# Optimization experiments

Measured on AMD Instinct MI355X. Metric: run time of the kernel, lower is better.

## Reference

```python
import jax, jax.numpy as jnp
import numpy as np

N, NFEAT, NHID, E = 100000, 256, 64, 1600000
EPS = 1e-5
NEG_SLOPE = 0.2


def _glorot(k, shape):
    lim = float(np.sqrt(6.0 / (shape[0] + shape[1])))
    return jax.random.uniform(k, shape, jnp.float32, -lim, lim)


def setup_inputs() -> dict:
    key = jax.random.key(0)
    ks = jax.random.split(key, 24)
    inp = {
        "g": jax.random.normal(ks[0], (N, NFEAT), jnp.float32),           # node features
        "x": jax.random.randint(ks[1], (2, E), 0, N),                      # edge_index [src; dst]
    }
    # estimator GAT params
    inp["est_W"] = _glorot(ks[2], (NFEAT, NHID))
    inp["est_asrc"] = _glorot(ks[3], (NHID, 1))[:, 0]
    inp["est_adst"] = _glorot(ks[4], (NHID, 1))[:, 0]
    inp["est_bias"] = jnp.zeros((NHID,), jnp.float32)
    inp["est_gamma"] = jnp.ones((NHID,), jnp.float32)
    inp["est_beta"] = jnp.zeros((NHID,), jnp.float32)
    inp["est_rmean"] = 0.1 * jax.random.normal(ks[5], (NHID,), jnp.float32)
    inp["est_rvar"] = jax.random.uniform(ks[6], (NHID,), jnp.float32, 0.5, 1.5)
    # GNN GAT params
    inp["gnn_W"] = _glorot(ks[7], (NFEAT, NHID))
    inp["gnn_asrc"] = _glorot(ks[8], (NHID, 1))[:, 0]
    inp["gnn_adst"] = _glorot(ks[9], (NHID, 1))[:, 0]
    inp["gnn_bias"] = jnp.zeros((NHID,), jnp.float32)
    inp["gnn_gamma"] = jnp.ones((NHID,), jnp.float32)
    inp["gnn_beta"] = jnp.zeros((NHID,), jnp.float32)
    inp["gnn_rmean"] = 0.1 * jax.random.normal(ks[10], (NHID,), jnp.float32)
    inp["gnn_rvar"] = jax.random.uniform(ks[11], (NHID,), jnp.float32, 0.5, 1.5)
    # classifier head
    inp["cls_W"] = _glorot(ks[12], (NHID, 1))
    inp["cls_b"] = jnp.zeros((1,), jnp.float32)
    return inp


def _gat(feat, src, dst, W, a_src, a_dst, bias, gamma, beta, rmean, rvar):
    # GATConv (heads=1): linear -> per-edge attention logits -> segment softmax over dst -> weighted scatter
    h = feat @ W                                  # [N, NHID]
    e_src = h @ a_src                             # [N]
    e_dst = h @ a_dst                             # [N]
    e = jax.nn.leaky_relu(e_src[src] + e_dst[dst], NEG_SLOPE)   # [E+N]
    m = jax.ops.segment_max(e, dst, num_segments=N)
    p = jnp.exp(e - m[dst])
    z = jax.ops.segment_sum(p, dst, num_segments=N)
    alpha = p / z[dst]                            # softmax per destination node
    out = jax.ops.segment_sum(h[src] * alpha[:, None], dst, num_segments=N) + bias
    # transition: ReLU -> BatchNorm1d (eval, running stats) -> Dropout (identity in eval)
    out = jnp.maximum(out, 0.0)
    return (out - rmean) * jax.lax.rsqrt(rvar + EPS) * gamma + beta


def reference(g, x, est_W, est_asrc, est_adst, est_bias, est_gamma, est_beta, est_rmean, est_rvar,
              gnn_W, gnn_asrc, gnn_adst, gnn_bias, gnn_gamma, gnn_beta, gnn_rmean, gnn_rvar,
              cls_W, cls_b):
    loop = jnp.arange(N)                          # add_self_loops=True
    src = jnp.concatenate([x[0], loop])
    dst = jnp.concatenate([x[1], loop])
    s = _gat(g, src, dst, est_W, est_asrc, est_adst, est_bias, est_gamma, est_beta, est_rmean, est_rvar)
    z = _gat(g, src, dst, gnn_W, gnn_asrc, gnn_adst, gnn_bias, gnn_gamma, gnn_beta, gnn_rmean, gnn_rvar)
    y = z @ cls_W + cls_b                         # [N, 1]
    return (y, s)
```

## Files before the change

kernel.cpp:

```cpp
#include <hip/hip_runtime.h>
#include <math.h>
#include <float.h>

#define NFEAT 256
#define NHID 64
#define BN_EPS 1e-5f

typedef float f32x4 __attribute__((ext_vector_type(4)));
typedef short s16x8 __attribute__((ext_vector_type(8)));

__device__ __forceinline__ float lrelu(float x) { return x >= 0.f ? x : 0.2f * x; }
__device__ __forceinline__ unsigned short f2bf(float f) {
    unsigned int u = __float_as_uint(f);
    return (unsigned short)((u + 0x7fffu + ((u >> 16) & 1u)) >> 16);
}
__device__ __forceinline__ float bf_lo(unsigned int v) { return __uint_as_float(v << 16); }
__device__ __forceinline__ float bf_hi(unsigned int v) { return __uint_as_float(v & 0xffff0000u); }

__global__ void prep_w_k(const float* __restrict__ We, const float* __restrict__ Wg,
                         unsigned short* __restrict__ Wt) {
    int tid = blockIdx.x * 256 + threadIdx.x;
    int ks  = tid >> 12;
    int col = (tid >> 5) & 127;
    int kk  = tid & 31;
    int k   = ks * 32 + kk;
    float v = (col < 64) ? We[k * 64 + col] : Wg[k * 64 + (col - 64)];
    size_t byte = (size_t)ks * 10240 + col * 80 + (kk >> 3) * 16 + (kk & 7) * 2;
    Wt[byte >> 1] = f2bf(v);
}

__global__ void bucket_hist_k(const int* __restrict__ x, int E, int* __restrict__ bcnt) {
    __shared__ int lh[256];
    int tid = threadIdx.x;
    lh[tid] = 0;
    __syncthreads();
    int base = (blockIdx.x * 256 + tid) * 8;
    if (base + 8 <= E) {
        int4 d0 = *(const int4*)(x + E + base);
        int4 d1 = *(const int4*)(x + E + base + 4);
        atomicAdd(&lh[d0.x >> 9], 1); atomicAdd(&lh[d0.y >> 9], 1);
        atomicAdd(&lh[d0.z >> 9], 1); atomicAdd(&lh[d0.w >> 9], 1);
        atomicAdd(&lh[d1.x >> 9], 1); atomicAdd(&lh[d1.y >> 9], 1);
        atomicAdd(&lh[d1.z >> 9], 1); atomicAdd(&lh[d1.w >> 9], 1);
    } else {
        for (int k = 0; k < 8; ++k)
            if (base + k < E) atomicAdd(&lh[x[E + base + k] >> 9], 1);
    }
    __syncthreads();
    if (lh[tid] > 0) atomicAdd(&bcnt[tid], lh[tid]);
}

__global__ void bucket_scan_k(const int* __restrict__ bcnt, int M, int NBKT,
                              int* __restrict__ bucket_base, int* __restrict__ bcursor,
                              int* __restrict__ csr_base) {
    __shared__ int s_c[2][256], s_t[2][256];
    int tid = threadIdx.x;
    int c = (tid < NBKT) ? bcnt[tid] : 0;
    int n0 = tid << 9;
    int sc = (tid < NBKT) ? min(512, M - n0) : 0;
    int tot = c + sc;
    s_c[0][tid] = c; s_t[0][tid] = tot;
    __syncthreads();
    int cur = 0;
    for (int off = 1; off < 256; off <<= 1) {
        int nc = s_c[cur][tid] + (tid >= off ? s_c[cur][tid - off] : 0);
        int nt = s_t[cur][tid] + (tid >= off ? s_t[cur][tid - off] : 0);
        s_c[cur ^ 1][tid] = nc; s_t[cur ^ 1][tid] = nt;
        __syncthreads();
        cur ^= 1;
    }
    if (tid < NBKT) {
        int eb = s_c[cur][tid] - c;
        bucket_base[tid] = eb;
        bcursor[tid] = eb;
        csr_base[tid] = s_t[cur][tid] - tot;
    }
}

__global__ void bucket_scatter_k(const int* __restrict__ x, int E,
                                 int* __restrict__ bcursor, int* __restrict__ ebuf) {
    __shared__ int lh[256], gb[256];
    int tid = threadIdx.x;
    lh[tid] = 0;
    __syncthreads();
    int base = (blockIdx.x * 256 + tid) * 8;
    int pk[8], bk[8], rk[8];
    bool v[8];
    if (base + 8 <= E) {
        int4 s0 = *(const int4*)(x + base);
        int4 s1 = *(const int4*)(x + base + 4);
        int4 d0 = *(const int4*)(x + E + base);
        int4 d1 = *(const int4*)(x + E + base + 4);
        int ss[8] = {s0.x, s0.y, s0.z, s0.w, s1.x, s1.y, s1.z, s1.w};
        int dd[8] = {d0.x, d0.y, d0.z, d0.w, d1.x, d1.y, d1.z, d1.w};
#pragma unroll
        for (int k = 0; k < 8; ++k) {
            v[k] = true;
            bk[k] = dd[k] >> 9;
            pk[k] = ((dd[k] & 511) << 17) | ss[k];
        }
    } else {
#pragma unroll
        for (int k = 0; k < 8; ++k) {
            int i = base + k;
            v[k] = (i < E);
            if (v[k]) {
                int s = x[i], d = x[E + i];
                bk[k] = d >> 9;
                pk[k] = ((d & 511) << 17) | s;
            } else { bk[k] = 0; pk[k] = 0; }
        }
    }
#pragma unroll
    for (int k = 0; k < 8; ++k)
        if (v[k]) rk[k] = atomicAdd(&lh[bk[k]], 1);
    __syncthreads();
    if (lh[tid] > 0) gb[tid] = atomicAdd(&bcursor[tid], lh[tid]);
    __syncthreads();
#pragma unroll
    for (int k = 0; k < 8; ++k)
        if (v[k]) ebuf[gb[bk[k]] + rk[k]] = pk[k];
}

__global__ __launch_bounds__(256) void bucket_csr_k(const int* __restrict__ bcnt,
                                                    const int* __restrict__ bucket_base,
                                                    const int* __restrict__ csr_base,
                                                    const int* __restrict__ ebuf, int M,
                                                    int* __restrict__ row_start,
                                                    int* __restrict__ deg,
                                                    int* __restrict__ srcs) {
    int b = blockIdx.x, tid = threadIdx.x;
    int nE = bcnt[b];
    int ebase = bucket_base[b];
    int cbase = csr_base[b];
    int n0 = b << 9;
    int nloc = min(512, M - n0);
    __shared__ int cnt[512], sa[512], sb[512], cur[512];
#pragma unroll
    for (int k = 0; k < 2; ++k) {
        int i = tid + k * 256;
        cnt[i] = (i < nloc) ? 1 : 0;
    }
    __syncthreads();
    for (int j = tid; j < nE; j += 256)
        atomicAdd(&cnt[ebuf[ebase + j] >> 17], 1);
    __syncthreads();
#pragma unroll
    for (int k = 0; k < 2; ++k) { int i = tid + k * 256; sa[i] = cnt[i]; }
    __syncthreads();
    int* a = sa; int* bb = sb;
    for (int off = 1; off < 512; off <<= 1) {
#pragma unroll
        for (int k = 0; k < 2; ++k) {
            int i = tid + k * 256;
            bb[i] = a[i] + (i >= off ? a[i - off] : 0);
        }
        __syncthreads();
        int* t = a; a = bb; bb = t;
    }
#pragma unroll
    for (int k = 0; k < 2; ++k) {
        int i = tid + k * 256;
        int excl = a[i] - cnt[i];
        cur[i] = excl;
        if (i < nloc) {
            row_start[n0 + i] = cbase + excl;
            deg[n0 + i] = cnt[i];
            srcs[cbase + excl] = n0 + i;
            cur[i] = excl + 1;
        }
    }
    __syncthreads();
    for (int j = tid; j < nE; j += 256) {
        int p = ebuf[ebase + j];
        int dl = p >> 17, src = p & 0x1FFFF;
        int pos = atomicAdd(&cur[dl], 1);
        srcs[cbase + pos] = src;
    }
}

__global__ __launch_bounds__(256) void gemm_mfma_k(const float* __restrict__ g,
                                                   const char* __restrict__ Wt,
                                                   unsigned short* __restrict__ hh,
                                                   const float* __restrict__ ase,
                                                   const float* __restrict__ ade,
                                                   const float* __restrict__ asg,
                                                   const float* __restrict__ adg,
                                                   float2* __restrict__ esrc,
                                                   float2* __restrict__ edst, int M) {
    __shared__ __align__(16) char lds[21504];
    char* As = lds;
    char* Bs = lds + 10240;
    float* av = (float*)(lds + 20480);
    const int tid = threadIdx.x;
    const int l = tid & 63;
    const int w = tid >> 6;
    const int row0 = blockIdx.x * 128;

    {
        float v;
        if (tid < 64)       v = ase[tid];
        else if (tid < 128) v = ade[tid - 64];
        else if (tid < 192) v = asg[tid - 128];
        else                v = adg[tid - 192];
        av[tid] = v;
    }

    f32x4 acc[2][8];
#pragma unroll
    for (int r = 0; r < 2; r++)
#pragma unroll
        for (int n = 0; n < 8; n++) acc[r][n] = (f32x4){0.f, 0.f, 0.f, 0.f};

    const int arow = tid >> 1;
    const int ah = tid & 1;

    for (int ks = 0; ks < 8; ++ks) {
        {
            int grow = row0 + arow;
            float4 v0 = {0,0,0,0}, v1 = v0, v2 = v0, v3 = v0;
            if (grow < M) {
                const float* gp = g + (size_t)grow * NFEAT + ks * 32 + ah * 16;
                v0 = *(const float4*)(gp + 0);
                v1 = *(const float4*)(gp + 4);
                v2 = *(const float4*)(gp + 8);
                v3 = *(const float4*)(gp + 12);
            }
            s16x8 c0, c1;
            c0[0]=f2bf(v0.x); c0[1]=f2bf(v0.y); c0[2]=f2bf(v0.z); c0[3]=f2bf(v0.w);
            c0[4]=f2bf(v1.x); c0[5]=f2bf(v1.y); c0[6]=f2bf(v1.z); c0[7]=f2bf(v1.w);
            c1[0]=f2bf(v2.x); c1[1]=f2bf(v2.y); c1[2]=f2bf(v2.z); c1[3]=f2bf(v2.w);
            c1[4]=f2bf(v3.x); c1[5]=f2bf(v3.y); c1[6]=f2bf(v3.z); c1[7]=f2bf(v3.w);
            *(s16x8*)(As + arow * 80 + ah * 32)      = c0;
            *(s16x8*)(As + arow * 80 + ah * 32 + 16) = c1;
        }
        {
            const char* wp = Wt + (size_t)ks * 10240 + arow * 80 + ah * 32;
            *(s16x8*)(Bs + arow * 80 + ah * 32)      = *(const s16x8*)(wp);
            *(s16x8*)(Bs + arow * 80 + ah * 32 + 16) = *(const s16x8*)(wp + 16);
        }
        __syncthreads();
        s16x8 af[2];
#pragma unroll
        for (int r = 0; r < 2; r++)
            af[r] = *(const s16x8*)(As + (w * 32 + r * 16 + (l & 15)) * 80 + (l >> 4) * 16);
#pragma unroll
        for (int n = 0; n < 8; n++) {
            s16x8 bf = *(const s16x8*)(Bs + (n * 16 + (l & 15)) * 80 + (l >> 4) * 16);
            acc[0][n] = __builtin_amdgcn_mfma_f32_16x16x32_bf16(af[0], bf, acc[0][n], 0, 0, 0);
            acc[1][n] = __builtin_amdgcn_mfma_f32_16x16x32_bf16(af[1], bf, acc[1][n], 0, 0, 0);
        }
        __syncthreads();
    }

    float vs_e[4], vd_e[4], vs_g[4], vd_g[4];
    {
        const int l16 = l & 15;
#pragma unroll
        for (int n = 0; n < 4; ++n) {
            vs_e[n] = av[n * 16 + l16];
            vd_e[n] = av[64 + n * 16 + l16];
            vs_g[n] = av[128 + n * 16 + l16];
            vd_g[n] = av[192 + n * 16 + l16];
        }
    }

    unsigned short* epi = (unsigned short*)lds;
#pragma unroll
    for (int p = 0; p < 2; ++p) {
        {
            float pse[4] = {0,0,0,0}, pde[4] = {0,0,0,0};
            float psg[4] = {0,0,0,0}, pdg[4] = {0,0,0,0};
#pragma unroll
            for (int n = 0; n < 4; ++n)
#pragma unroll
                for (int j = 0; j < 4; ++j) {
                    float he = acc[p][n][j];
                    float hg = acc[p][n + 4][j];
                    pse[j] += he * vs_e[n];
                    pde[j] += he * vd_e[n];
                    psg[j] += hg * vs_g[n];
                    pdg[j] += hg * vd_g[n];
                }
#pragma unroll
            for (int off = 1; off <= 8; off <<= 1) {
#pragma unroll
                for (int j = 0; j < 4; ++j) {
                    pse[j] += __shfl_xor(pse[j], off, 64);
                    pde[j] += __shfl_xor(pde[j], off, 64);
                    psg[j] += __shfl_xor(psg[j], off, 64);
                    pdg[j] += __shfl_xor(pdg[j], off, 64);
                }
            }
            if ((l & 15) == 0) {
#pragma unroll
                for (int j = 0; j < 4; ++j) {
                    int gr = row0 + w * 32 + p * 16 + (l >> 4) * 4 + j;
                    if (gr < M) {
                        esrc[gr] = make_float2(pse[j], psg[j]);
                        edst[gr] = make_float2(pde[j], pdg[j]);
                    }
                }
            }
        }
#pragma unroll
        for (int n = 0; n < 8; n++)
#pragma unroll
            for (int j = 0; j < 4; j++)
                epi[(w * 16 + (l >> 4) * 4 + j) * 128 + n * 16 + (l & 15)] = f2bf(acc[p][n][j]);
        __syncthreads();
        int er = tid >> 2, sgm = tid & 3;
        int grow2 = row0 + 32 * (er >> 4) + 16 * p + (er & 15);
        if (grow2 < M) {
            const s16x8* src = (const s16x8*)(epi + er * 128 + sgm * 32);
            s16x8* dst = (s16x8*)(hh + (size_t)grow2 * 128 + sgm * 32);
#pragma unroll
            for (int q = 0; q < 4; q++) dst[q] = src[q];
        }
        __syncthreads();
    }
}

__global__ void node_acc_k(const int* __restrict__ srcs, const int* __restrict__ row_start,
                           const int* __restrict__ deg,
                           const float2* __restrict__ esrc, const float2* __restrict__ edst,
                           const unsigned short* __restrict__ hh,
                           const float* __restrict__ be, const float* __restrict__ ge,
                           const float* __restrict__ bte, const float* __restrict__ rme,
                           const float* __restrict__ rve,
                           const float* __restrict__ bg, const float* __restrict__ gg,
                           const float* __restrict__ btg, const float* __restrict__ rmg,
                           const float* __restrict__ rvg,
                           const float* __restrict__ clsW, const float* __restrict__ clsb,
                           float* __restrict__ y, float* __restrict__ s_out, int M) {
    int n = blockIdx.x * 4 + (threadIdx.x >> 6);
    int l = threadIdx.x & 63;
    if (n >= M) return;
    int beg = row_start[n];
    int cnt = deg[n];
    int eh = l >> 5;
    int li = l & 31;
    int layer = li >> 4;
    float2 ed = edst[n];
    float edv = layer ? ed.y : ed.x;
    const int* sp = srcs + beg;
    const char* hb = (const char*)hh + (unsigned)li * 8;
    float a0 = 0.f, a1 = 0.f, a2 = 0.f, a3 = 0.f, zacc = 0.f;
    int j = 0;
    for (; j + 8 <= cnt; j += 8) {
        int s[4];
#pragma unroll
        for (int k = 0; k < 4; ++k) s[k] = sp[j + 2 * k + eh];
        float2 e[4];
        uint2 h[4];
#pragma unroll
        for (int k = 0; k < 4; ++k) e[k] = esrc[s[k]];
#pragma unroll
        for (int k = 0; k < 4; ++k)
            h[k] = *(const uint2*)(hb + ((size_t)(unsigned)s[k] << 8));
#pragma unroll
        for (int k = 0; k < 4; ++k) {
            float a = __expf(lrelu((layer ? e[k].y : e[k].x) + edv));
            zacc += a;
            a0 += a * bf_lo(h[k].x); a1 += a * bf_hi(h[k].x);
            a2 += a * bf_lo(h[k].y); a3 += a * bf_hi(h[k].y);
        }
    }
    for (; j < cnt; j += 2) {
        int idx = j + eh;
        if (idx < cnt) {
            int s = sp[idx];
            float2 e = esrc[s];
            uint2 h = *(const uint2*)(hb + ((size_t)(unsigned)s << 8));
            float a = __expf(lrelu((layer ? e.y : e.x) + edv));
            zacc += a;
            a0 += a * bf_lo(h.x); a1 += a * bf_hi(h.x);
            a2 += a * bf_lo(h.y); a3 += a * bf_hi(h.y);
        }
    }
    a0 += __shfl_xor(a0, 32, 64);
    a1 += __shfl_xor(a1, 32, 64);
    a2 += __shfl_xor(a2, 32, 64);
    a3 += __shfl_xor(a3, 32, 64);
    zacc += __shfl_xor(zacc, 32, 64);
    float rz = 1.f / zacc;
    float o0 = a0 * rz, o1 = a1 * rz, o2 = a2 * rz, o3 = a3 * rz;

    int c16 = li & 15;
    float4 b4  = layer ? ((const float4*)bg)[c16]  : ((const float4*)be)[c16];
    float4 rm4 = layer ? ((const float4*)rmg)[c16] : ((const float4*)rme)[c16];
    float4 rv4 = layer ? ((const float4*)rvg)[c16] : ((const float4*)rve)[c16];
    float4 g4  = layer ? ((const float4*)gg)[c16]  : ((const float4*)ge)[c16];
    float4 bt4 = layer ? ((const float4*)btg)[c16] : ((const float4*)bte)[c16];
    o0 = (fmaxf(o0 + b4.x, 0.f) - rm4.x) * rsqrtf(rv4.x + BN_EPS) * g4.x + bt4.x;
    o1 = (fmaxf(o1 + b4.y, 0.f) - rm4.y) * rsqrtf(rv4.y + BN_EPS) * g4.y + bt4.y;
    o2 = (fmaxf(o2 + b4.z, 0.f) - rm4.z) * rsqrtf(rv4.z + BN_EPS) * g4.z + bt4.z;
    o3 = (fmaxf(o3 + b4.w, 0.f) - rm4.w) * rsqrtf(rv4.w + BN_EPS) * g4.w + bt4.w;

    if (eh == 0) {
        if (layer == 0) {
            float4 sv = {o0, o1, o2, o3};
            ((float4*)(s_out + (size_t)n * 64))[c16] = sv;
        } else {
            float4 w4 = ((const float4*)clsW)[c16];
            float t = o0 * w4.x + o1 * w4.y + o2 * w4.z + o3 * w4.w;
#pragma unroll
            for (int off = 1; off <= 8; off <<= 1) t += __shfl_xor(t, off, 64);
            if (li == 16) y[n] = t + clsb[0];
        }
    }
}

extern "C" void kernel_launch(void* const* d_in, const int* in_sizes, int n_in,
                              void* d_out, int out_size, void* d_ws, size_t ws_size,
                              hipStream_t stream) {
    const float* g        = (const float*)d_in[0];
    const int*   x        = (const int*)d_in[1];
    const float* est_W    = (const float*)d_in[2];
    const float* est_asrc = (const float*)d_in[3];
    const float* est_adst = (const float*)d_in[4];
    const float* est_bias = (const float*)d_in[5];
    const float* est_gamma= (const float*)d_in[6];
    const float* est_beta = (const float*)d_in[7];
    const float* est_rmean= (const float*)d_in[8];
    const float* est_rvar = (const float*)d_in[9];
    const float* gnn_W    = (const float*)d_in[10];
    const float* gnn_asrc = (const float*)d_in[11];
    const float* gnn_adst = (const float*)d_in[12];
    const float* gnn_bias = (const float*)d_in[13];
    const float* gnn_gamma= (const float*)d_in[14];
    const float* gnn_beta = (const float*)d_in[15];
    const float* gnn_rmean= (const float*)d_in[16];
    const float* gnn_rvar = (const float*)d_in[17];
    const float* cls_W    = (const float*)d_in[18];
    const float* cls_b    = (const float*)d_in[19];

    const int M  = in_sizes[0] / NFEAT;
    const int E  = in_sizes[1] / 2;
    const int Et = E + M;
    const int NBKT = (M + 511) >> 9;

    float* y_out = (float*)d_out;
    float* s_out = y_out + M;

    char* base = (char*)d_ws;
    unsigned short* hh = (unsigned short*)base;
    size_t off = (size_t)M * 128 * 2;
    char* Wt = base + off;                  off += 81920;
    float2* esrc = (float2*)(base + off);   off += (size_t)M * 8;
    float2* edst = (float2*)(base + off);   off += (size_t)M * 8;
    int* deg       = (int*)(base + off);    off += (size_t)M * 4;
    int* row_start = (int*)(base + off);    off += (size_t)M * 4;
    int* srcs      = (int*)(base + off);    off += (size_t)Et * 4;
    int* ebuf      = (int*)(base + off);    off += (size_t)E * 4;
    int* bcnt        = (int*)(base + off);  off += 256 * 4;
    int* bucket_base = (int*)(base + off);  off += 256 * 4;
    int* bcursor     = (int*)(base + off);  off += 256 * 4;
    int* csr_base    = (int*)(base + off);  off += 256 * 4;

    const int EB = (E + 2047) / 2048;

    prep_w_k<<<128, 256, 0, stream>>>(est_W, gnn_W, (unsigned short*)Wt);
    hipMemsetAsync(bcnt, 0, 256 * 4, stream);
    bucket_hist_k<<<EB, 256, 0, stream>>>(x, E, bcnt);
    bucket_scan_k<<<1, 256, 0, stream>>>(bcnt, M, NBKT, bucket_base, bcursor, csr_base);
    bucket_scatter_k<<<EB, 256, 0, stream>>>(x, E, bcursor, ebuf);
    bucket_csr_k<<<NBKT, 256, 0, stream>>>(bcnt, bucket_base, csr_base, ebuf, M,
                                           row_start, deg, srcs);

    gemm_mfma_k<<<(M + 127) / 128, 256, 0, stream>>>(g, Wt, hh,
                                                     est_asrc, est_adst, gnn_asrc, gnn_adst,
                                                     esrc, edst, M);

    node_acc_k<<<(M + 3) / 4, 256, 0, stream>>>(srcs, row_start, deg, esrc, edst, hh,
                                                est_bias, est_gamma, est_beta, est_rmean, est_rvar,
                                                gnn_bias, gnn_gamma, gnn_beta, gnn_rmean, gnn_rvar,
                                                cls_W, cls_b, y_out, s_out, M);
}
```

Before: 201.1 us.

## Precompute per-edge attention weights during CSR construction and reorder GEMM first

Moves the GEMM ahead of the CSR build so that bucket_csr_k can compute exp(leaky_relu(esrc+edst)) for both layers per edge. It writes these into a new CSR-ordered pa array. node_acc_k then streams pa sequentially instead of gathering esrc randomly and recomputing exp. This replaces a random 8-byte gather per edge with a coalesced read, but adds a random esrc gather and extra 8-byte writes in the CSR kernel.

```diff
diff --git a/kernel.cpp b/kernel.cpp
--- a/kernel.cpp
+++ b/kernel.cpp
@@ -126,9 +126,12 @@
                                                     const int* __restrict__ bucket_base,
                                                     const int* __restrict__ csr_base,
                                                     const int* __restrict__ ebuf, int M,
+                                                    const float2* __restrict__ esrc,
+                                                    const float2* __restrict__ edst,
                                                     int* __restrict__ row_start,
                                                     int* __restrict__ deg,
-                                                    int* __restrict__ srcs) {
+                                                    int* __restrict__ srcs,
+                                                    float2* __restrict__ pa) {
     int b = blockIdx.x, tid = threadIdx.x;
     int nE = bcnt[b];
     int ebase = bucket_base[b];
@@ -136,10 +139,12 @@
     int n0 = b << 9;
     int nloc = min(512, M - n0);
     __shared__ int cnt[512], sa[512], sb[512], cur[512];
+    __shared__ float2 edl[512];
 #pragma unroll
     for (int k = 0; k < 2; ++k) {
         int i = tid + k * 256;
         cnt[i] = (i < nloc) ? 1 : 0;
+        edl[i] = (i < nloc) ? edst[n0 + i] : make_float2(0.f, 0.f);
     }
     __syncthreads();
     for (int j = tid; j < nE; j += 256)
@@ -167,6 +172,10 @@
             row_start[n0 + i] = cbase + excl;
             deg[n0 + i] = cnt[i];
             srcs[cbase + excl] = n0 + i;
+            float2 es = esrc[n0 + i];
+            float2 ed = edl[i];
+            pa[cbase + excl] = make_float2(__expf(lrelu(es.x + ed.x)),
+                                           __expf(lrelu(es.y + ed.y)));
             cur[i] = excl + 1;
         }
     }
@@ -176,6 +185,10 @@
         int dl = p >> 17, src = p & 0x1FFFF;
         int pos = atomicAdd(&cur[dl], 1);
         srcs[cbase + pos] = src;
+        float2 es = esrc[src];
+        float2 ed = edl[dl];
+        pa[cbase + pos] = make_float2(__expf(lrelu(es.x + ed.x)),
+                                      __expf(lrelu(es.y + ed.y)));
     }
 }
 
@@ -322,8 +335,7 @@
 }
 
 __global__ void node_acc_k(const int* __restrict__ srcs, const int* __restrict__ row_start,
-                           const int* __restrict__ deg,
-                           const float2* __restrict__ esrc, const float2* __restrict__ edst,
+                           const int* __restrict__ deg, const float2* __restrict__ pa,
                            const unsigned short* __restrict__ hh,
                            const float* __restrict__ be, const float* __restrict__ ge,
                            const float* __restrict__ bte, const float* __restrict__ rme,
@@ -341,26 +353,25 @@
     int eh = l >> 5;
     int li = l & 31;
     int layer = li >> 4;
-    float2 ed = edst[n];
-    float edv = layer ? ed.y : ed.x;
     const int* sp = srcs + beg;
+    const float2* pp = pa + beg;
     const char* hb = (const char*)hh + (unsigned)li * 8;
     float a0 = 0.f, a1 = 0.f, a2 = 0.f, a3 = 0.f, zacc = 0.f;
     int j = 0;
     for (; j + 8 <= cnt; j += 8) {
         int s[4];
+        float2 pv[4];
+        uint2 h[4];
 #pragma unroll
         for (int k = 0; k < 4; ++k) s[k] = sp[j + 2 * k + eh];
-        float2 e[4];
-        uint2 h[4];
-#pragma unroll
-        for (int k = 0; k < 4; ++k) e[k] = esrc[s[k]];
+#pragma unroll
+        for (int k = 0; k < 4; ++k) pv[k] = pp[j + 2 * k + eh];
 #pragma unroll
         for (int k = 0; k < 4; ++k)
             h[k] = *(const uint2*)(hb + ((size_t)(unsigned)s[k] << 8));
 #pragma unroll
         for (int k = 0; k < 4; ++k) {
-            float a = __expf(lrelu((layer ? e[k].y : e[k].x) + edv));
+            float a = layer ? pv[k].y : pv[k].x;
             zacc += a;
             a0 += a * bf_lo(h[k].x); a1 += a * bf_hi(h[k].x);
             a2 += a * bf_lo(h[k].y); a3 += a * bf_hi(h[k].y);
@@ -370,9 +381,9 @@
         int idx = j + eh;
         if (idx < cnt) {
             int s = sp[idx];
-            float2 e = esrc[s];
+            float2 pv = pp[idx];
             uint2 h = *(const uint2*)(hb + ((size_t)(unsigned)s << 8));
-            float a = __expf(lrelu((layer ? e.y : e.x) + edv));
+            float a = layer ? pv.y : pv.x;
             zacc += a;
             a0 += a * bf_lo(h.x); a1 += a * bf_hi(h.x);
             a2 += a * bf_lo(h.y); a3 += a * bf_hi(h.y);
@@ -452,6 +463,7 @@
     int* deg       = (int*)(base + off);    off += (size_t)M * 4;
     int* row_start = (int*)(base + off);    off += (size_t)M * 4;
     int* srcs      = (int*)(base + off);    off += (size_t)Et * 4;
+    float2* pa     = (float2*)(base + off); off += (size_t)Et * 8;
     int* ebuf      = (int*)(base + off);    off += (size_t)E * 4;
     int* bcnt        = (int*)(base + off);  off += 256 * 4;
     int* bucket_base = (int*)(base + off);  off += 256 * 4;
@@ -461,18 +473,18 @@
     const int EB = (E + 2047) / 2048;
 
     prep_w_k<<<128, 256, 0, stream>>>(est_W, gnn_W, (unsigned short*)Wt);
+    gemm_mfma_k<<<(M + 127) / 128, 256, 0, stream>>>(g, Wt, hh,
+                                                     est_asrc, est_adst, gnn_asrc, gnn_adst,
+                                                     esrc, edst, M);
+
     hipMemsetAsync(bcnt, 0, 256 * 4, stream);
     bucket_hist_k<<<EB, 256, 0, stream>>>(x, E, bcnt);
     bucket_scan_k<<<1, 256, 0, stream>>>(bcnt, M, NBKT, bucket_base, bcursor, csr_base);
     bucket_scatter_k<<<EB, 256, 0, stream>>>(x, E, bcursor, ebuf);
     bucket_csr_k<<<NBKT, 256, 0, stream>>>(bcnt, bucket_base, csr_base, ebuf, M,
-                                           row_start, deg, srcs);
-
-    gemm_mfma_k<<<(M + 127) / 128, 256, 0, stream>>>(g, Wt, hh,
-                                                     est_asrc, est_adst, gnn_asrc, gnn_adst,
-                                                     esrc, edst, M);
-
-    node_acc_k<<<(M + 3) / 4, 256, 0, stream>>>(srcs, row_start, deg, esrc, edst, hh,
+                                           esrc, edst, row_start, deg, srcs, pa);
+
+    node_acc_k<<<(M + 3) / 4, 256, 0, stream>>>(srcs, row_start, deg, pa, hh,
                                                 est_bias, est_gamma, est_beta, est_rmean, est_rvar,
                                                 gnn_bias, gnn_gamma, gnn_beta, gnn_rmean, gnn_rvar,
                                                 cls_W, cls_b, y_out, s_out, M);
```

New measurement: 270.5 us. 1.35x slower.
